# Optimization experiments

Hardware: AMD Instinct MI355X
Metric: run time of the kernel (lower is better)

## Reference

```python
import jax, jax.numpy as jnp
import numpy as np

S, B, F, H = 4096, 32, 512, 512


def setup_inputs() -> dict:
    key = jax.random.key(0)
    k1, k2, k3, k4 = jax.random.split(key, 4)
    features = jax.random.normal(k1, (S, B, F), dtype=jnp.float32)
    hidden = jax.random.normal(k2, (1, B, H), dtype=jnp.float32)
    # binary padding mask (1 = masked-out position)
    mask = (jax.random.uniform(k3, (S, B)) < 0.1).astype(jnp.float32)
    W_key = jax.random.normal(k4, (H, F), dtype=jnp.float32) * 0.02
    b_key = jnp.zeros((H,), dtype=jnp.float32)
    return {"features": features, "hidden": hidden, "mask": mask,
            "W_key": W_key, "b_key": b_key}


def reference(features, hidden, mask, W_key, b_key):
    # key projection: [S,B,F] @ [F,H] -> [S,B,H]
    k = jnp.einsum('sbf,hf->sbh', features, W_key) + b_key
    # score = <key, hidden> per (s,b); hidden broadcasts over seq
    scores = jnp.einsum('sbh,bh->sb', k, hidden[0]) + mask * -99999.0
    # softmax over the sequence axis (dim 0)
    distribution = jax.nn.softmax(scores, axis=0)  # [S,B]
    # weighted-sum pooling of the ORIGINAL features
    summary = jnp.einsum('sbf,sb->bf', features, distribution)[None]  # [1,B,F]
    return summary, distribution
```

## Files before the change

kernel.cpp:

```cpp
#include <hip/hip_runtime.h>

constexpr int S = 4096;
constexpr int B = 32;
constexpr int F = 512;
constexpr int H = 512;

__global__ void proj_kernel(const float* __restrict__ hidden,
                            const float* __restrict__ W_key,
                            float* __restrict__ v) {
    const int b = blockIdx.y;
    const int f = blockIdx.x * 64 + threadIdx.x;
    const float* hb = hidden + b * H;
    float acc = 0.f;
#pragma unroll 8
    for (int h = 0; h < H; ++h)
        acc = fmaf(hb[h], W_key[h * F + f], acc);
    v[b * F + f] = acc;
}

__global__ void bias_dot_kernel(const float* __restrict__ hidden,
                                const float* __restrict__ b_key,
                                float* __restrict__ c) {
    const int b = blockIdx.x;
    const int lane = threadIdx.x;
    float acc = 0.f;
    for (int h = lane; h < H; h += 64)
        acc = fmaf(b_key[h], hidden[b * H + h], acc);
    for (int off = 32; off; off >>= 1) acc += __shfl_down(acc, off);
    if (lane == 0) c[b] = acc;
}

__global__ void score_kernel(const float* __restrict__ features,
                             const float* __restrict__ mask,
                             const float* __restrict__ v,
                             const float* __restrict__ c,
                             float* __restrict__ scores) {
    const int wid = (blockIdx.x * blockDim.x + threadIdx.x) >> 6;
    const int lane = threadIdx.x & 63;
    const int s = wid / B;
    const int b = wid - s * B;

    const float4* row = reinterpret_cast<const float4*>(features + (size_t)wid * F);
    const float4* vb  = reinterpret_cast<const float4*>(v + b * F);

    float4 r0 = row[lane];
    float4 r1 = row[lane + 64];
    float4 v0 = vb[lane];
    float4 v1 = vb[lane + 64];

    float acc = r0.x * v0.x + r0.y * v0.y + r0.z * v0.z + r0.w * v0.w
              + r1.x * v1.x + r1.y * v1.y + r1.z * v1.z + r1.w * v1.w;

    for (int off = 32; off; off >>= 1) acc += __shfl_down(acc, off);

    if (lane == 0)
        scores[wid] = acc + c[b] - 99999.0f * mask[wid];
}

__global__ void softmax_kernel(const float* __restrict__ scores,
                               float* __restrict__ dist) {
    const int b = blockIdx.x;
    const int t = threadIdx.x;
    __shared__ float sm[S];
    __shared__ float red[256];

    float m = -1e30f;
    for (int s = t; s < S; s += 256) {
        float x = scores[s * B + b];
        sm[s] = x;
        m = fmaxf(m, x);
    }
    red[t] = m;
    __syncthreads();
    for (int off = 128; off; off >>= 1) {
        if (t < off) red[t] = fmaxf(red[t], red[t + off]);
        __syncthreads();
    }
    m = red[0];
    __syncthreads();

    float sum = 0.f;
    for (int s = t; s < S; s += 256) {
        float e = expf(sm[s] - m);
        sm[s] = e;
        sum += e;
    }
    red[t] = sum;
    __syncthreads();
    for (int off = 128; off; off >>= 1) {
        if (t < off) red[t] += red[t + off];
        __syncthreads();
    }
    const float inv = 1.f / red[0];

    for (int s = t; s < S; s += 256)
        dist[s * B + b] = sm[s] * inv;
}

constexpr int POOL_CHUNK = 128;

__global__ void pool_kernel(const float* __restrict__ features,
                            const float* __restrict__ dist,
                            float* __restrict__ summary) {
    const int b = blockIdx.x;
    const int chunk = blockIdx.y;
    const int f = threadIdx.x;
    const int s0 = chunk * POOL_CHUNK;

    float acc = 0.f;
    for (int s = s0; s < s0 + POOL_CHUNK; ++s) {
        const float w = dist[s * B + b];
        acc = fmaf(w, features[((size_t)s * B + b) * F + f], acc);
    }
    atomicAdd(&summary[b * F + f], acc);
}

extern "C" void kernel_launch(void* const* d_in, const int* in_sizes, int n_in,
                              void* d_out, int out_size, void* d_ws, size_t ws_size,
                              hipStream_t stream) {
    const float* features = (const float*)d_in[0];
    const float* hidden   = (const float*)d_in[1];
    const float* mask     = (const float*)d_in[2];
    const float* W_key    = (const float*)d_in[3];
    const float* b_key    = (const float*)d_in[4];

    float* out     = (float*)d_out;
    float* summary = out;
    float* dist    = out + B * F;

    float* v      = (float*)d_ws;
    float* c      = v + B * F;
    float* scores = c + 32;

    hipMemsetAsync(summary, 0, B * F * sizeof(float), stream);

    proj_kernel<<<dim3(F / 64, B), 64, 0, stream>>>(hidden, W_key, v);
    bias_dot_kernel<<<B, 64, 0, stream>>>(hidden, b_key, c);
    score_kernel<<<(S * B) / 4, 256, 0, stream>>>(features, mask, v, c, scores);
    softmax_kernel<<<B, 256, 0, stream>>>(scores, dist);
    pool_kernel<<<dim3(B, S / POOL_CHUNK), 512, 0, stream>>>(features, dist, summary);
}
```

Baseline: 451.4 us.

## Fuse score and pooling with online softmax to read features once

Replaces the separate score, softmax and pool kernels with one kernel. Each wave processes 32 sequence rows for one batch, computes the scores and keeps an online-softmax running max, sum and weighted feature accumulator. Small combine, dist and summary kernels then merge the per-chunk partials. This removes the second full pass over the 256MB features tensor, at the cost of a partial-accumulator buffer in workspace and extra exp/rescale work per row.

New measurement: 413.0 us. 1.09x faster.

```diff
diff --git a/kernel.cpp b/kernel.cpp
--- a/kernel.cpp
+++ b/kernel.cpp
@@ -4,6 +4,10 @@
 constexpr int B = 32;
 constexpr int F = 512;
 constexpr int H = 512;
+
+constexpr int RPW    = 32;
+constexpr int CHUNKS = S / RPW;
+constexpr int WPB    = 4;
 
 __global__ void proj_kernel(const float* __restrict__ hidden,
                             const float* __restrict__ W_key,
@@ -30,87 +34,147 @@
     if (lane == 0) c[b] = acc;
 }
 
-__global__ void score_kernel(const float* __restrict__ features,
-                             const float* __restrict__ mask,
-                             const float* __restrict__ v,
-                             const float* __restrict__ c,
-                             float* __restrict__ scores) {
-    const int wid = (blockIdx.x * blockDim.x + threadIdx.x) >> 6;
-    const int lane = threadIdx.x & 63;
-    const int s = wid / B;
-    const int b = wid - s * B;
-
-    const float4* row = reinterpret_cast<const float4*>(features + (size_t)wid * F);
-    const float4* vb  = reinterpret_cast<const float4*>(v + b * F);
-
+__global__ __launch_bounds__(WPB * 64) void fused_score_pool(
+    const float* __restrict__ features,
+    const float* __restrict__ mask,
+    const float* __restrict__ v,
+    const float* __restrict__ c,
+    float* __restrict__ scores,
+    float* __restrict__ pacc,
+    float* __restrict__ pm,
+    float* __restrict__ pl) {
+    const int lane  = threadIdx.x & 63;
+    const int b     = blockIdx.x & (B - 1);
+    const int chunk = (blockIdx.x >> 5) * WPB + (threadIdx.x >> 6);
+    const int s0    = chunk * RPW;
+
+    const float4* vb = reinterpret_cast<const float4*>(v + b * F);
+    const float4 v0 = vb[lane];
+    const float4 v1 = vb[lane + 64];
+    const float cb = c[b];
+
+    float m = -3.0e38f, l = 0.f;
+    float4 a0 = make_float4(0.f, 0.f, 0.f, 0.f);
+    float4 a1 = make_float4(0.f, 0.f, 0.f, 0.f);
+
+    const float4* row = reinterpret_cast<const float4*>(
+        features + ((size_t)s0 * B + b) * F);
     float4 r0 = row[lane];
     float4 r1 = row[lane + 64];
-    float4 v0 = vb[lane];
-    float4 v1 = vb[lane + 64];
-
-    float acc = r0.x * v0.x + r0.y * v0.y + r0.z * v0.z + r0.w * v0.w
-              + r1.x * v1.x + r1.y * v1.y + r1.z * v1.z + r1.w * v1.w;
-
-    for (int off = 32; off; off >>= 1) acc += __shfl_down(acc, off);
-
-    if (lane == 0)
-        scores[wid] = acc + c[b] - 99999.0f * mask[wid];
-}
-
-__global__ void softmax_kernel(const float* __restrict__ scores,
-                               float* __restrict__ dist) {
+    float mk = mask[s0 * B + b];
+
+    for (int i = 0; i < RPW; ++i) {
+        const int sn = s0 + ((i + 1 < RPW) ? i + 1 : i);
+        const float4* nrow = reinterpret_cast<const float4*>(
+            features + ((size_t)sn * B + b) * F);
+        float4 n0 = nrow[lane];
+        float4 n1 = nrow[lane + 64];
+        float nmk = mask[sn * B + b];
+
+        float dot = r0.x * v0.x + r0.y * v0.y + r0.z * v0.z + r0.w * v0.w
+                  + r1.x * v1.x + r1.y * v1.y + r1.z * v1.z + r1.w * v1.w;
+#pragma unroll
+        for (int off = 32; off; off >>= 1) dot += __shfl_xor(dot, off);
+
+        const float score = dot + cb - 99999.0f * mk;
+        if (lane == 0) scores[(s0 + i) * B + b] = score;
+
+        if (score > m) {
+            const float sc = __expf(m - score);
+            a0.x = fmaf(a0.x, sc, r0.x);
+            a0.y = fmaf(a0.y, sc, r0.y);
+            a0.z = fmaf(a0.z, sc, r0.z);
+            a0.w = fmaf(a0.w, sc, r0.w);
+            a1.x = fmaf(a1.x, sc, r1.x);
+            a1.y = fmaf(a1.y, sc, r1.y);
+            a1.z = fmaf(a1.z, sc, r1.z);
+            a1.w = fmaf(a1.w, sc, r1.w);
+            l = fmaf(l, sc, 1.f);
+            m = score;
+        } else {
+            const float w = __expf(score - m);
+            a0.x = fmaf(w, r0.x, a0.x);
+            a0.y = fmaf(w, r0.y, a0.y);
+            a0.z = fmaf(w, r0.z, a0.z);
+            a0.w = fmaf(w, r0.w, a0.w);
+            a1.x = fmaf(w, r1.x, a1.x);
+            a1.y = fmaf(w, r1.y, a1.y);
+            a1.z = fmaf(w, r1.z, a1.z);
+            a1.w = fmaf(w, r1.w, a1.w);
+            l += w;
+        }
+        r0 = n0; r1 = n1; mk = nmk;
+    }
+
+    float4* pa = reinterpret_cast<float4*>(pacc + ((size_t)b * CHUNKS + chunk) * F);
+    pa[lane]      = a0;
+    pa[lane + 64] = a1;
+    if (lane == 0) {
+        pm[b * CHUNKS + chunk] = m;
+        pl[b * CHUNKS + chunk] = l;
+    }
+}
+
+__global__ void combine_kernel(const float* __restrict__ pm,
+                               const float* __restrict__ pl,
+                               float* __restrict__ Mb,
+                               float* __restrict__ invLb) {
     const int b = blockIdx.x;
     const int t = threadIdx.x;
-    __shared__ float sm[S];
-    __shared__ float red[256];
-
-    float m = -1e30f;
-    for (int s = t; s < S; s += 256) {
-        float x = scores[s * B + b];
-        sm[s] = x;
-        m = fmaxf(m, x);
-    }
-    red[t] = m;
+    __shared__ float sm[CHUNKS];
+    __shared__ float sl[CHUNKS];
+
+    const float mv = pm[b * CHUNKS + t];
+    sm[t] = mv;
     __syncthreads();
-    for (int off = 128; off; off >>= 1) {
-        if (t < off) red[t] = fmaxf(red[t], red[t + off]);
+    for (int off = CHUNKS / 2; off; off >>= 1) {
+        if (t < off) sm[t] = fmaxf(sm[t], sm[t + off]);
         __syncthreads();
     }
-    m = red[0];
+    const float M = sm[0];
     __syncthreads();
 
-    float sum = 0.f;
-    for (int s = t; s < S; s += 256) {
-        float e = expf(sm[s] - m);
-        sm[s] = e;
-        sum += e;
-    }
-    red[t] = sum;
+    sl[t] = pl[b * CHUNKS + t] * __expf(mv - M);
     __syncthreads();
-    for (int off = 128; off; off >>= 1) {
-        if (t < off) red[t] += red[t + off];
+    for (int off = CHUNKS / 2; off; off >>= 1) {
+        if (t < off) sl[t] += sl[t + off];
         __syncthreads();
     }
-    const float inv = 1.f / red[0];
-
-    for (int s = t; s < S; s += 256)
-        dist[s * B + b] = sm[s] * inv;
-}
-
-constexpr int POOL_CHUNK = 128;
-
-__global__ void pool_kernel(const float* __restrict__ features,
-                            const float* __restrict__ dist,
-                            float* __restrict__ summary) {
+    if (t == 0) {
+        Mb[b] = M;
+        invLb[b] = 1.f / sl[0];
+    }
+}
+
+__global__ void dist_kernel(const float* __restrict__ scores,
+                            const float* __restrict__ Mb,
+                            const float* __restrict__ invLb,
+                            float* __restrict__ dist) {
+    const int i = blockIdx.x * blockDim.x + threadIdx.x;
+    const int b = i & (B - 1);
+    dist[i] = __expf(scores[i] - Mb[b]) * invLb[b];
+}
+
+constexpr int QCH = CHUNKS / 4;
+
+__global__ __launch_bounds__(F) void summary_kernel(
+    const float* __restrict__ pacc,
+    const float* __restrict__ pm,
+    const float* __restrict__ Mb,
+    const float* __restrict__ invLb,
+    float* __restrict__ summary) {
     const int b = blockIdx.x;
-    const int chunk = blockIdx.y;
+    const int q = blockIdx.y;
     const int f = threadIdx.x;
-    const int s0 = chunk * POOL_CHUNK;
+    const float M = Mb[b];
+    const float invL = invLb[b];
 
     float acc = 0.f;
-    for (int s = s0; s < s0 + POOL_CHUNK; ++s) {
-        const float w = dist[s * B + b];
-        acc = fmaf(w, features[((size_t)s * B + b) * F + f], acc);
+#pragma unroll 4
+    for (int j = 0; j < QCH; ++j) {
+        const int cidx = q * QCH + j;
+        const float coef = __expf(pm[b * CHUNKS + cidx] - M) * invL;
+        acc = fmaf(coef, pacc[((size_t)b * CHUNKS + cidx) * F + f], acc);
     }
     atomicAdd(&summary[b * F + f], acc);
 }
@@ -128,15 +192,25 @@
     float* summary = out;
     float* dist    = out + B * F;
 
-    float* v      = (float*)d_ws;
+    float* ws     = (float*)d_ws;
+    float* pacc   = ws;
+    float* v      = pacc + (size_t)B * CHUNKS * F;
     float* c      = v + B * F;
-    float* scores = c + 32;
+    float* Mb     = c + B;
+    float* invLb  = Mb + B;
+    float* pm     = invLb + B;
+    float* pl     = pm + B * CHUNKS;
+    float* scores = pl + B * CHUNKS;
 
     hipMemsetAsync(summary, 0, B * F * sizeof(float), stream);
 
     proj_kernel<<<dim3(F / 64, B), 64, 0, stream>>>(hidden, W_key, v);
     bias_dot_kernel<<<B, 64, 0, stream>>>(hidden, b_key, c);
-    score_kernel<<<(S * B) / 4, 256, 0, stream>>>(features, mask, v, c, scores);
-    softmax_kernel<<<B, 256, 0, stream>>>(scores, dist);
-    pool_kernel<<<dim3(B, S / POOL_CHUNK), 512, 0, stream>>>(features, dist, summary);
-}
+
+    fused_score_pool<<<B * CHUNKS / WPB, WPB * 64, 0, stream>>>(
+        features, mask, v, c, scores, pacc, pm, pl);
+
+    combine_kernel<<<B, CHUNKS, 0, stream>>>(pm, pl, Mb, invLb);
+    dist_kernel<<<(S * B) / 256, 256, 0, stream>>>(scores, Mb, invLb, dist);
+    summary_kernel<<<dim3(B, 4), F, 0, stream>>>(pacc, pm, Mb, invLb, summary);
+}
```
